# Kernel tuning notes

Hardware: AMD Instinct MI355X
Metric: run time of the kernel (lower is better)

## Reference

```python
import jax, jax.numpy as jnp
import numpy as np

B, N, E, H = 8, 512, 256, 8
HD = E // H
FF = 4 * E
TOPK = max(1, int(N * 0.2))
FW_MAX_DIST = 10      # default of get_shortest_path_matrix
EMB_MAX_IDX = 6       # spd encoder: max_dist(5) + 1
LN_EPS = 1e-5


def _layernorm(x, g, b):
    m = jnp.mean(x, axis=-1, keepdims=True)
    v = jnp.var(x, axis=-1, keepdims=True)
    return (x - m) / jnp.sqrt(v + LN_EPS) * g + b


def setup_inputs() -> dict:
    key = jax.random.key(0)
    ks = jax.random.split(key, 12)
    s = 0.02
    return {
        "x": jax.random.normal(ks[0], (B, N, E), jnp.float32),
        "adj": jax.random.uniform(ks[1], (B, N, N), jnp.float32),
        "emb_spd": (jax.random.normal(ks[2], (EMB_MAX_IDX + 1, H), jnp.float32) * s),
        "w_qkv": jax.random.normal(ks[3], (3 * E, E), jnp.float32) * s,
        "b_qkv": jnp.zeros((3 * E,), jnp.float32),
        "w_out": jax.random.normal(ks[4], (E, E), jnp.float32) * s,
        "b_out": jnp.zeros((E,), jnp.float32),
        "w_ff1": jax.random.normal(ks[5], (FF, E), jnp.float32) * s,
        "b_ff1": jnp.zeros((FF,), jnp.float32),
        "w_ff2": jax.random.normal(ks[6], (E, FF), jnp.float32) * s,
        "b_ff2": jnp.zeros((E,), jnp.float32),
        "g1": jnp.ones((E,), jnp.float32),
        "beta1": jnp.zeros((E,), jnp.float32),
        "g2": jnp.ones((E,), jnp.float32),
        "beta2": jnp.zeros((E,), jnp.float32),
        "w_pool": jax.random.normal(ks[7], (1, E), jnp.float32) * s,
        "b_pool": jnp.zeros((1,), jnp.float32),
    }


def _combined_mask(adj, emb_spd):
    # top-k per row -> binary adjacency via scatter
    _, idx = jax.lax.top_k(adj, TOPK)                       # [B,N,k]
    bi = jnp.arange(B)[:, None, None]
    ri = jnp.arange(N)[None, :, None]
    binary = jnp.zeros_like(adj).at[bi, ri, idx].set(1.0)   # [B,N,N]

    # Floyd-Warshall shortest paths
    dist = jnp.where(binary == 1.0, 1.0, jnp.inf)
    ids = jnp.arange(N)
    dist = dist.at[:, ids, ids].set(0.0)

    def body(k, d):
        return jnp.minimum(d, d[:, :, k][:, :, None] + d[:, k, :][:, None, :])

    dist = jax.lax.fori_loop(0, N, body, dist)
    dist_i = jnp.where(dist > FW_MAX_DIST, -1.0, dist).astype(jnp.int32)

    # spatial bias embedding: indices = clamp(dist+1, 0, max_dist+1)
    sp_idx = jnp.clip(dist_i + 1, 0, EMB_MAX_IDX)           # [B,N,N]
    bias = jnp.transpose(emb_spd[sp_idx], (0, 3, 1, 2))     # [B,H,N,N]

    base = jnp.where(binary == 0.0, -jnp.inf, 0.0)[:, None] # [B,1,N,N]
    return base + bias                                      # [B,H,N,N]


def reference(x, adj, emb_spd, w_qkv, b_qkv, w_out, b_out,
              w_ff1, b_ff1, w_ff2, b_ff2, g1, beta1, g2, beta2,
              w_pool, b_pool):
    mask = _combined_mask(adj, emb_spd)                     # [B,H,N,N]

    # multi-head self-attention (PyTorch MHA, post-norm encoder layer, eval)
    qkv = x @ w_qkv.T + b_qkv                               # [B,N,3E]
    q, k, v = jnp.split(qkv, 3, axis=-1)
    q = q.reshape(B, N, H, HD).transpose(0, 2, 1, 3)
    k = k.reshape(B, N, H, HD).transpose(0, 2, 1, 3)
    v = v.reshape(B, N, H, HD).transpose(0, 2, 1, 3)
    scores = jnp.einsum("bhqd,bhkd->bhqk", q, k) / np.sqrt(HD) + mask
    attn = jax.nn.softmax(scores, axis=-1)
    ctx = jnp.einsum("bhqk,bhkd->bhqd", attn, v)
    ctx = ctx.transpose(0, 2, 1, 3).reshape(B, N, E)
    attn_out = ctx @ w_out.T + b_out

    x1 = _layernorm(x + attn_out, g1, beta1)
    ff = jax.nn.relu(x1 @ w_ff1.T + b_ff1) @ w_ff2.T + b_ff2
    x2 = _layernorm(x1 + ff, g2, beta2)

    # attention pooling over nodes
    w = jax.nn.softmax(jnp.tanh(x2 @ w_pool.T + b_pool), axis=1)  # [B,N,1]
    return jnp.sum(x2 * w, axis=1)                          # [B,E]
```

## Files before the change

kernel.cpp:

```cpp
#include <hip/hip_runtime.h>
#include <math.h>


#define B_ 8
#define N_ 512
#define E_ 256
#define H_ 8
#define HD_ 32
#define TOPK_ 102

typedef __attribute__((ext_vector_type(8))) short bf16x8;
typedef __attribute__((ext_vector_type(4))) float f32x4;

__device__ __forceinline__ unsigned short f2b(float f) {
  unsigned u = __builtin_bit_cast(unsigned, f);
  return (unsigned short)((u + 0x7FFFu + ((u >> 16) & 1u)) >> 16);
}

__device__ __forceinline__ uint4 lnpack(const float* __restrict__ p,
                                        const float* __restrict__ g,
                                        const float* __restrict__ b,
                                        float mean, float inv) {
  float4 v0 = *(const float4*)p, v1 = *(const float4*)(p + 4);
  float4 g0 = *(const float4*)g, g1 = *(const float4*)(g + 4);
  float4 b0 = *(const float4*)b, b1 = *(const float4*)(b + 4);
  unsigned short h0 = f2b((v0.x - mean) * inv * g0.x + b0.x);
  unsigned short h1 = f2b((v0.y - mean) * inv * g0.y + b0.y);
  unsigned short h2 = f2b((v0.z - mean) * inv * g0.z + b0.z);
  unsigned short h3 = f2b((v0.w - mean) * inv * g0.w + b0.w);
  unsigned short h4 = f2b((v1.x - mean) * inv * g1.x + b1.x);
  unsigned short h5 = f2b((v1.y - mean) * inv * g1.y + b1.y);
  unsigned short h6 = f2b((v1.z - mean) * inv * g1.z + b1.z);
  unsigned short h7 = f2b((v1.w - mean) * inv * g1.w + b1.w);
  uint4 u;
  u.x = (unsigned)h0 | ((unsigned)h1 << 16);
  u.y = (unsigned)h2 | ((unsigned)h3 << 16);
  u.z = (unsigned)h4 | ((unsigned)h5 << 16);
  u.w = (unsigned)h6 | ((unsigned)h7 << 16);
  return u;
}

__global__ __launch_bounds__(256) void cvt_topk(
    const float* __restrict__ adj, unsigned int* __restrict__ bits,
    const float* __restrict__ x, const float* __restrict__ wqkv,
    const float* __restrict__ wout, const float* __restrict__ wff1,
    const float* __restrict__ wff2, unsigned short* __restrict__ xb,
    unsigned short* __restrict__ wqkvb, unsigned short* __restrict__ woutb,
    unsigned short* __restrict__ wff1b, unsigned short* __restrict__ wff2b,
    float* __restrict__ rstat) {
  __shared__ unsigned int hist[1024];
  __shared__ float cval[64];
  __shared__ int cidx[64];
  __shared__ int s_cnt, s_bb, s_need;
  __shared__ unsigned int rowbits[16];
  __shared__ int wsum[4];
  const int t = threadIdx.x;

  if (blockIdx.x >= 5888) {
    int i4 = (blockIdx.x - 5888) * 1024 + t * 4;
    *(float4*)(rstat + i4) = (float4){0.f, 0.f, 0.f, 0.f};
    return;
  }
  if (blockIdx.x >= 4096) {
    int i = ((blockIdx.x - 4096) * 256 + t) * 4;
    const float* src;
    unsigned short* dst;
    int off;
    if (i < 1048576)      { src = x;    dst = xb;    off = i; }
    else if (i < 1245184) { src = wqkv; dst = wqkvb; off = i - 1048576; }
    else if (i < 1310720) { src = wout; dst = woutb; off = i - 1245184; }
    else if (i < 1572864) { src = wff1; dst = wff1b; off = i - 1310720; }
    else                  { src = wff2; dst = wff2b; off = i - 1572864; }
    float4 v = *(const float4*)(src + off);
    ushort4 o;
    o.x = f2b(v.x); o.y = f2b(v.y); o.z = f2b(v.z); o.w = f2b(v.w);
    *(ushort4*)(dst + off) = o;
    return;
  }
  const int row = blockIdx.x;
  const float* a = adj + (size_t)row * N_;
  const int lane = t & 63;
  const int wave = t >> 6;

  hist[t] = 0u; hist[t + 256] = 0u; hist[t + 512] = 0u; hist[t + 768] = 0u;
  if (t == 0) s_cnt = 0;
  float v0 = a[t];
  float v1 = a[t + 256];
  __syncthreads();
  const int b0 = min(1023, max(0, (int)(v0 * 1024.0f)));
  const int b1 = min(1023, max(0, (int)(v1 * 1024.0f)));
  atomicAdd(&hist[b0], 1u);
  atomicAdd(&hist[b1], 1u);
  __syncthreads();
  const int base = 1020 - 4 * t;
  const int h0 = (int)hist[base], h1 = (int)hist[base + 1];
  const int h2 = (int)hist[base + 2], h3 = (int)hist[base + 3];
  const int g = h0 + h1 + h2 + h3;
  int sc = g;
  #pragma unroll
  for (int off = 1; off < 64; off <<= 1) {
    int y = __shfl_up(sc, off);
    sc += (lane >= off) ? y : 0;
  }
  if (lane == 63) wsum[wave] = sc;
  __syncthreads();
  int wo = 0;
  for (int w = 0; w < wave; w++) wo += wsum[w];
  const int incl = sc + wo;
  const int excl = incl - g;
  if (excl < TOPK_ && incl >= TOPK_) {
    int cum = excl;
    int bb = base;
    const int hh[4] = {h3, h2, h1, h0};
    const int bs[4] = {base + 3, base + 2, base + 1, base};
    #pragma unroll
    for (int u = 0; u < 4; u++) {
      if (cum + hh[u] >= TOPK_) { bb = bs[u]; break; }
      cum += hh[u];
    }
    s_bb = bb;
    s_need = TOPK_ - cum;
  }
  __syncthreads();
  const int bb = s_bb;
  const int need = s_need;
  const bool sel0 = (b0 > bb);
  const bool sel1 = (b1 > bb);
  if (b0 == bb) { int p = atomicAdd(&s_cnt, 1); if (p < 64) { cval[p] = v0; cidx[p] = t; } }
  if (b1 == bb) { int p = atomicAdd(&s_cnt, 1); if (p < 64) { cval[p] = v1; cidx[p] = t + 256; } }
  unsigned long long m0 = __ballot(sel0);
  unsigned long long m1 = __ballot(sel1);
  if (lane == 0) {
    rowbits[2 * wave + 0] = (unsigned int)m0;
    rowbits[2 * wave + 1] = (unsigned int)(m0 >> 32);
    rowbits[8 + 2 * wave + 0] = (unsigned int)m1;
    rowbits[8 + 2 * wave + 1] = (unsigned int)(m1 >> 32);
  }
  __syncthreads();
  const int cnt = min(s_cnt, 64);
  for (int c = t; c < cnt; c += 256) {
    const float v = cval[c];
    const int idx = cidx[c];
    int r = 0;
    for (int j = 0; j < cnt; j++) {
      const float vj = cval[j];
      const int ij = cidx[j];
      if (vj > v || (vj == v && ij < idx)) r++;
    }
    if (r < need) atomicOr(&rowbits[idx >> 5], 1u << (idx & 31));
  }
  __syncthreads();
  if (t < 16) bits[(size_t)row * 16 + t] = rowbits[t];
}

template <int FLAGS>
__global__ __launch_bounds__(256) void gemm_mfma(
    const unsigned short* __restrict__ A, const float* __restrict__ A32,
    const unsigned short* __restrict__ W, const float* __restrict__ bias,
    const float* __restrict__ res, void* __restrict__ Cout,
    unsigned short* __restrict__ kG, unsigned short* __restrict__ vG,
    float* __restrict__ rstat, const float* __restrict__ lng,
    const float* __restrict__ lnb, int M, int N, int K) {
  __shared__ __align__(16) unsigned short Af[8 * 64 * 8];
  __shared__ __align__(16) unsigned short Wf[8 * 64 * 8];
  const int tid = threadIdx.x;
  const int m0 = blockIdx.y * 64, n0 = blockIdx.x * 64;
  const int wave = tid >> 6, lane = tid & 63;
  const int wm = wave & 1, wn = wave >> 1;
  const int q = lane >> 4, l15 = lane & 15;
  const int r = tid >> 2, c0 = tid & 3;

  f32x4 acc[2][2];
  #pragma unroll
  for (int i = 0; i < 2; i++)
    #pragma unroll
    for (int j = 0; j < 2; j++) acc[i][j] = (f32x4){0.f, 0.f, 0.f, 0.f};

  float lmean = 0.f, linv = 0.f;
  if (FLAGS & 16) {
    float s = rstat[(size_t)(m0 + r) * 2];
    float s2 = rstat[(size_t)(m0 + r) * 2 + 1];
    lmean = s * (1.f / 256.f);
    float var = s2 * (1.f / 256.f) - lmean * lmean;
    linv = rsqrtf(var + 1e-5f);
  }

  const size_t arow = (size_t)(m0 + r) * K;
  const size_t wrow = (size_t)(n0 + r) * K;
  for (int k0 = 0; k0 < K; k0 += 64) {
    uint4 a0, a1;
    if (FLAGS & 16) {
      a0 = lnpack(A32 + arow + k0 + c0 * 8, lng + k0 + c0 * 8,
                  lnb + k0 + c0 * 8, lmean, linv);
      a1 = lnpack(A32 + arow + k0 + (c0 + 4) * 8, lng + k0 + (c0 + 4) * 8,
                  lnb + k0 + (c0 + 4) * 8, lmean, linv);
    } else {
      a0 = *(const uint4*)(A + arow + k0 + c0 * 8);
      a1 = *(const uint4*)(A + arow + k0 + (c0 + 4) * 8);
    }
    uint4 w0 = *(const uint4*)(W + wrow + k0 + c0 * 8);
    uint4 w1 = *(const uint4*)(W + wrow + k0 + (c0 + 4) * 8);
    __syncthreads();
    {
      int kc = c0 >> 2, qq = c0 & 3;
      int s0 = ((r >> 4) * 2 + kc) * 64 + (r & 15) + qq * 16;
      int kc1 = (c0 + 4) >> 2, qq1 = (c0 + 4) & 3;
      int s1 = ((r >> 4) * 2 + kc1) * 64 + (r & 15) + qq1 * 16;
      *(uint4*)(Af + s0 * 8) = a0;
      *(uint4*)(Af + s1 * 8) = a1;
      *(uint4*)(Wf + s0 * 8) = w0;
      *(uint4*)(Wf + s1 * 8) = w1;
    }
    __syncthreads();
    #pragma unroll
    for (int kc = 0; kc < 2; kc++) {
      bf16x8 af[2], wf[2];
      #pragma unroll
      for (int mt = 0; mt < 2; mt++)
        af[mt] = *(const bf16x8*)(Af + (((wm * 2 + mt) * 2 + kc) * 64 + lane) * 8);
      #pragma unroll
      for (int nt = 0; nt < 2; nt++)
        wf[nt] = *(const bf16x8*)(Wf + (((wn * 2 + nt) * 2 + kc) * 64 + lane) * 8);
      #pragma unroll
      for (int mt = 0; mt < 2; mt++)
        #pragma unroll
        for (int nt = 0; nt < 2; nt++)
          acc[mt][nt] = __builtin_amdgcn_mfma_f32_16x16x32_bf16(af[mt], wf[nt], acc[mt][nt], 0, 0, 0);
    }
  }
  float srow[2][4], sqrow[2][4];
  if (FLAGS & 8) {
    #pragma unroll
    for (int mt = 0; mt < 2; mt++)
      #pragma unroll
      for (int reg = 0; reg < 4; reg++) { srow[mt][reg] = 0.f; sqrow[mt][reg] = 0.f; }
  }
  #pragma unroll
  for (int nt = 0; nt < 2; nt++) {
    const int col = n0 + (wn * 2 + nt) * 16 + l15;
    const float bv = bias[col];
    #pragma unroll
    for (int mt = 0; mt < 2; mt++) {
      const int rowb = m0 + (wm * 2 + mt) * 16 + q * 4;
      float ov[4];
      #pragma unroll
      for (int reg = 0; reg < 4; reg++) {
        float o = acc[mt][nt][reg] + bv;
        if (res) {
          float rv = res[(size_t)(rowb + reg) * N + col];
          if (FLAGS & 32) {
            const int rr = rowb + reg;
            float s = rstat[(size_t)rr * 2];
            float s2 = rstat[(size_t)rr * 2 + 1];
            float mn = s * (1.f / 256.f);
            float vv = s2 * (1.f / 256.f) - mn * mn;
            float iv = rsqrtf(vv + 1e-5f);
            rv = (rv - mn) * iv * lng[col] + lnb[col];
          }
          o += rv;
        }
        if (FLAGS & 1) o = fmaxf(o, 0.f);
        if (FLAGS & 8) { srow[mt][reg] += o; sqrow[mt][reg] += o * o; }
        ov[reg] = o;
      }
      if (FLAGS & 4) {
        if (col < 256) {
          #pragma unroll
          for (int reg = 0; reg < 4; reg++)
            ((unsigned short*)Cout)[(size_t)(rowb + reg) * 256 + col] = f2b(ov[reg]);
        } else if (col < 512) {
          const int dfull = col - 256;
          const int hh2 = dfull >> 5, d = dfull & 31;
          const int q2 = d >> 3, sub = d & 7;
          const int bidx = rowb >> 9, j = rowb & 511;
          const int jt = j >> 6, jtile = (j >> 4) & 3, jl = j & 15;
          unsigned short* kp = kG +
              ((size_t)(((bidx * 8 + hh2) * 8 + jt) * 4 + jtile) * 64 + q2 * 16 + jl) * 8 + sub;
          kp[0] = f2b(ov[0]); kp[8] = f2b(ov[1]); kp[16] = f2b(ov[2]); kp[24] = f2b(ov[3]);
        } else {
          const int dfull = col - 512;
          const int hh2 = dfull >> 5, d = dfull & 31;
          const int dt = d >> 4, dl = d & 15;
          const int bidx = rowb >> 9, j = rowb & 511;
          const int jt = j >> 6, jj = j & 63;
          const int kc = jj >> 5, q2 = (jj >> 3) & 3, sub0 = jj & 7;
          ushort4 st;
          st.x = f2b(ov[0]); st.y = f2b(ov[1]); st.z = f2b(ov[2]); st.w = f2b(ov[3]);
          *(ushort4*)(vG +
              ((size_t)(((bidx * 8 + hh2) * 8 + jt) * 4 + dt * 2 + kc) * 64 + q2 * 16 + dl) * 8 + sub0) = st;
        }
      } else if (FLAGS & 2) {
        #pragma unroll
        for (int reg = 0; reg < 4; reg++)
          ((unsigned short*)Cout)[(size_t)(rowb + reg) * N + col] = f2b(ov[reg]);
      } else {
        #pragma unroll
        for (int reg = 0; reg < 4; reg++)
          ((float*)Cout)[(size_t)(rowb + reg) * N + col] = ov[reg];
      }
    }
  }
  if (FLAGS & 8) {
    #pragma unroll
    for (int mt = 0; mt < 2; mt++)
      #pragma unroll
      for (int reg = 0; reg < 4; reg++) {
        float s = srow[mt][reg], s2 = sqrow[mt][reg];
        #pragma unroll
        for (int off = 1; off < 16; off <<= 1) {
          s += __shfl_xor(s, off);
          s2 += __shfl_xor(s2, off);
        }
        if (l15 == 0) {
          const int row = m0 + (wm * 2 + mt) * 16 + q * 4 + reg;
          atomicAdd(&rstat[(size_t)row * 2], s);
          atomicAdd(&rstat[(size_t)row * 2 + 1], s2);
        }
      }
  }
}

__global__ __launch_bounds__(256) void attn_mfma(
    const unsigned short* __restrict__ qb, const unsigned short* __restrict__ kG,
    const unsigned short* __restrict__ vG, const unsigned int* __restrict__ bits,
    const float* __restrict__ emb, unsigned short* __restrict__ ctxo) {
  const int bx = blockIdx.x;
  const int ib = bx & 7;
  const int h = (bx >> 3) & 7;
  const int b = bx >> 6;
  const int tid = threadIdx.x;
  const int lane = tid & 63;
  const int wave = tid >> 6;
  const int q = lane >> 4, l15 = lane & 15;

  __shared__ __align__(16) unsigned int mrow[64 * 16];
  __shared__ __align__(16) unsigned short pF[4][2 * 64 * 8];

  {
    int rr = tid >> 2, wq = tid & 3;
    uint4 mw = *(const uint4*)(bits + ((size_t)(b * N_ + ib * 64 + rr)) * 16 + wq * 4);
    *(uint4*)(mrow + rr * 16 + wq * 4) = mw;
  }
  __syncthreads();

  const int i0w = ib * 64 + wave * 16;
  const bf16x8 qf = *(const bf16x8*)(qb + ((size_t)(b * N_ + i0w + l15)) * 256 + h * HD_ + q * 8);
  const float delta = emb[1 * H_ + h] - emb[2 * H_ + h];
  const float scale = 0.17677669529663687f;

  float m_run[4], l_run[4];
  #pragma unroll
  for (int e = 0; e < 4; e++) { m_run[e] = -1e30f; l_run[e] = 0.f; }
  f32x4 cacc[2];
  cacc[0] = (f32x4){0.f, 0.f, 0.f, 0.f};
  cacc[1] = (f32x4){0.f, 0.f, 0.f, 0.f};

  unsigned short* pbase = &pF[wave][0];
  const unsigned short* kb = kG + (size_t)(b * 8 + h) * 8 * 4 * 512;
  const unsigned short* vb = vG + (size_t)(b * 8 + h) * 8 * 4 * 512;

  #pragma unroll 1
  for (int jt = 0; jt < 8; jt++) {
    f32x4 s4[4];
    #pragma unroll
    for (int jtile = 0; jtile < 4; jtile++) {
      bf16x8 kf = *(const bf16x8*)(kb + (size_t)(jt * 4 + jtile) * 512 + lane * 8);
      s4[jtile] = __builtin_amdgcn_mfma_f32_16x16x32_bf16(qf, kf, (f32x4){0.f, 0.f, 0.f, 0.f}, 0, 0, 0);
    }
    unsigned long long mw64[4];
    #pragma unroll
    for (int reg = 0; reg < 4; reg++)
      mw64[reg] = *(const unsigned long long*)(mrow + (wave * 16 + q * 4 + reg) * 16 + jt * 2);
    float smat[4][4];
    #pragma unroll
    for (int jtile = 0; jtile < 4; jtile++) {
      #pragma unroll
      for (int reg = 0; reg < 4; reg++) {
        unsigned int w = (jtile & 2) ? (unsigned int)(mw64[reg] >> 32) : (unsigned int)mw64[reg];
        bool allowed = ((w >> ((jtile & 1) * 16 + l15)) & 1u) != 0u;
        int ig = ib * 64 + wave * 16 + q * 4 + reg;
        int jg = jt * 64 + jtile * 16 + l15;
        float s = s4[jtile][reg] * scale + ((jg == ig) ? delta : 0.f);
        smat[jtile][reg] = allowed ? s : -INFINITY;
      }
    }
    float alpha[4], pmat[4][4];
    #pragma unroll
    for (int reg = 0; reg < 4; reg++) {
      float mloc = fmaxf(fmaxf(smat[0][reg], smat[1][reg]), fmaxf(smat[2][reg], smat[3][reg]));
      #pragma unroll
      for (int off = 1; off < 16; off <<= 1) mloc = fmaxf(mloc, __shfl_xor(mloc, off));
      float mnew = fmaxf(m_run[reg], mloc);
      alpha[reg] = __expf(m_run[reg] - mnew);
      m_run[reg] = mnew;
      float ps = 0.f;
      #pragma unroll
      for (int jtile = 0; jtile < 4; jtile++) {
        float p = __expf(smat[jtile][reg] - mnew);
        pmat[jtile][reg] = p;
        ps += p;
      }
      #pragma unroll
      for (int off = 1; off < 16; off <<= 1) ps += __shfl_xor(ps, off);
      l_run[reg] = l_run[reg] * alpha[reg] + ps;
      cacc[0][reg] *= alpha[reg];
      cacc[1][reg] *= alpha[reg];
    }
    #pragma unroll
    for (int jtile = 0; jtile < 4; jtile++) {
      int j_l = jtile * 16 + l15;
      int sl = ((j_l >> 5) * 64 + ((j_l >> 3) & 3) * 16) * 8 + (j_l & 7);
      #pragma unroll
      for (int reg = 0; reg < 4; reg++)
        pbase[sl + (q * 4 + reg) * 8] = f2b(pmat[jtile][reg]);
    }
    #pragma unroll
    for (int kc = 0; kc < 2; kc++) {
      bf16x8 pf = *(const bf16x8*)(pbase + (kc * 64 + lane) * 8);
      #pragma unroll
      for (int dt = 0; dt < 2; dt++) {
        bf16x8 vf = *(const bf16x8*)(vb + (size_t)(jt * 4 + dt * 2 + kc) * 512 + lane * 8);
        cacc[dt] = __builtin_amdgcn_mfma_f32_16x16x32_bf16(pf, vf, cacc[dt], 0, 0, 0);
      }
    }
  }
  #pragma unroll
  for (int reg = 0; reg < 4; reg++) {
    const float linv = 1.f / l_run[reg];
    const size_t row = (size_t)(b * N_ + i0w + q * 4 + reg);
    #pragma unroll
    for (int dt = 0; dt < 2; dt++)
      ctxo[row * E_ + h * HD_ + dt * 16 + l15] = f2b(cacc[dt][reg] * linv);
  }
}

__global__ __launch_bounds__(256) void ln2pool_kernel(
    const float* __restrict__ t, const float* __restrict__ g,
    const float* __restrict__ be, const float* __restrict__ wp,
    const float* __restrict__ bp, float* __restrict__ partial,
    float* __restrict__ pwsum) {
  __shared__ float sh[8];
  const int tid = threadIdx.x;
  const int wave = tid >> 6, lane = tid & 63;
  const int c = blockIdx.x;
  const float gv = g[tid], bev = be[tid], wpv = wp[tid], bpv = bp[0];
  float pacc = 0.f, esum = 0.f;
  #pragma unroll 1
  for (int rr = 0; rr < 8; rr++) {
    const int row = c * 8 + rr;
    float v = t[(size_t)row * E_ + tid];
    float s = v, s2 = v * v;
    #pragma unroll
    for (int off = 32; off > 0; off >>= 1) {
      s += __shfl_xor(s, off);
      s2 += __shfl_xor(s2, off);
    }
    __syncthreads();
    if (lane == 0) { sh[wave] = s; sh[4 + wave] = s2; }
    __syncthreads();
    s = sh[0] + sh[1] + sh[2] + sh[3];
    s2 = sh[4] + sh[5] + sh[6] + sh[7];
    float mean = s * (1.f / 256.f);
    float var = s2 * (1.f / 256.f) - mean * mean;
    float inv = rsqrtf(var + 1e-5f);
    float o = (v - mean) * inv * gv + bev;
    float d = o * wpv;
    #pragma unroll
    for (int off = 32; off > 0; off >>= 1) d += __shfl_xor(d, off);
    __syncthreads();
    if (lane == 0) sh[wave] = d;
    __syncthreads();
    float dot = sh[0] + sh[1] + sh[2] + sh[3] + bpv;
    float e = __expf(tanhf(dot));
    pacc += e * o;
    esum += e;
  }
  partial[(size_t)c * E_ + tid] = pacc;
  if (tid == 0) pwsum[c] = esum;
}

__global__ __launch_bounds__(256) void pool_final(
    const float* __restrict__ partial, const float* __restrict__ pwsum,
    float* __restrict__ out) {
  const int b = blockIdx.x;
  const int tid = threadIdx.x;
  float acc = 0.f, ws = 0.f;
  #pragma unroll
  for (int c = 0; c < 64; c++) acc += partial[(size_t)(b * 64 + c) * E_ + tid];
  #pragma unroll
  for (int c = 0; c < 64; c++) ws += pwsum[b * 64 + c];
  out[b * E_ + tid] = acc / ws;
}

extern "C" void kernel_launch(void* const* d_in, const int* in_sizes, int n_in,
                              void* d_out, int out_size, void* d_ws, size_t ws_size,
                              hipStream_t stream) {
  (void)in_sizes; (void)n_in; (void)out_size; (void)ws_size;
  const float* x      = (const float*)d_in[0];
  const float* adj    = (const float*)d_in[1];
  const float* emb    = (const float*)d_in[2];
  const float* w_qkv  = (const float*)d_in[3];
  const float* b_qkv  = (const float*)d_in[4];
  const float* w_out  = (const float*)d_in[5];
  const float* b_out  = (const float*)d_in[6];
  const float* w_ff1  = (const float*)d_in[7];
  const float* b_ff1  = (const float*)d_in[8];
  const float* w_ff2  = (const float*)d_in[9];
  const float* b_ff2  = (const float*)d_in[10];
  const float* g1     = (const float*)d_in[11];
  const float* be1    = (const float*)d_in[12];
  const float* g2     = (const float*)d_in[13];
  const float* be2    = (const float*)d_in[14];
  const float* w_pool = (const float*)d_in[15];
  const float* b_pool = (const float*)d_in[16];

  char* ws = (char*)d_ws;
  unsigned int*   bits  = (unsigned int*)ws;
  unsigned short* xb    = (unsigned short*)(ws + 262144);
  unsigned short* qb    = (unsigned short*)(ws + 2359296);
  unsigned short* kG    = (unsigned short*)(ws + 4456448);
  unsigned short* vG    = (unsigned short*)(ws + 6553600);
  unsigned short* ctxb  = (unsigned short*)(ws + 8650752);
  float*          tbuf  = (float*)(ws + 10747904);
  float*          tbuf2 = (float*)(ws + 14942208);
  float*          rstat = (float*)(ws + 19136512);
  unsigned short* hffb  = (unsigned short*)(ws + 21233664);
  unsigned short* wqkvb = (unsigned short*)(ws + 29622272);
  unsigned short* woutb = (unsigned short*)(ws + 30015488);
  unsigned short* wff1b = (unsigned short*)(ws + 30146560);
  unsigned short* wff2b = (unsigned short*)(ws + 30670848);
  float*          partial = (float*)(ws + 31195136);
  float*          pwsum   = (float*)(ws + 31719424);
  float*          outp  = (float*)d_out;

  const int M = B_ * N_;

  cvt_topk<<<4096 + 1792 + 2, 256, 0, stream>>>(
      adj, bits, x, w_qkv, w_out, w_ff1, w_ff2, xb, wqkvb, woutb, wff1b,
      wff2b, rstat);
  gemm_mfma<4><<<dim3(768 / 64, M / 64), 256, 0, stream>>>(
      xb, nullptr, wqkvb, b_qkv, nullptr, qb, kG, vG, nullptr, nullptr,
      nullptr, M, 768, E_);
  attn_mfma<<<B_ * H_ * (N_ / 64), 256, 0, stream>>>(qb, kG, vG, bits, emb, ctxb);
  gemm_mfma<8><<<dim3(E_ / 64, M / 64), 256, 0, stream>>>(
      ctxb, nullptr, woutb, b_out, x, tbuf, nullptr, nullptr, rstat, nullptr,
      nullptr, M, E_, E_);
  gemm_mfma<1 | 2 | 16><<<dim3(1024 / 64, M / 64), 256, 0, stream>>>(
      nullptr, tbuf, wff1b, b_ff1, nullptr, hffb, nullptr, nullptr, rstat,
      g1, be1, M, 1024, E_);
  gemm_mfma<32><<<dim3(E_ / 64, M / 64), 256, 0, stream>>>(
      hffb, nullptr, wff2b, b_ff2, tbuf, tbuf2, nullptr, nullptr, rstat,
      g1, be1, M, E_, 1024);
  ln2pool_kernel<<<M / 8, 256, 0, stream>>>(tbuf2, g2, be2, w_pool, b_pool,
                                            partial, pwsum);
  pool_final<<<B_, 256, 0, stream>>>(partial, pwsum, outp);
}
```

Before: 175.5 us.

## Use direct global-to-LDS loads in GEMM tiles and per-wave row pooling

The GEMM's bf16 A and W tile loads now use global_load_lds, so data goes straight from global memory into shared memory instead of passing through registers. The LDS layout is kept through per-lane address mapping. Runtime flag checks become if constexpr, and the residual path is gated by a new template bit rather than a null-pointer test. The LN2-plus-pool kernel now gives each wave whole rows with float4 loads and wave-level reductions, cutting the block barriers per row to a single final barrier. The risk is getting the LDS address mapping wrong for global_load_lds, and the GEMM still has no double buffering.

```diff
diff --git a/kernel.cpp b/kernel.cpp
--- a/kernel.cpp
+++ b/kernel.cpp
@@ -15,6 +15,12 @@
 __device__ __forceinline__ unsigned short f2b(float f) {
   unsigned u = __builtin_bit_cast(unsigned, f);
   return (unsigned short)((u + 0x7FFFu + ((u >> 16) & 1u)) >> 16);
+}
+
+__device__ __forceinline__ void gload16(const void* g, void* l) {
+  __builtin_amdgcn_global_load_lds(
+      (const __attribute__((address_space(1))) void*)g,
+      (__attribute__((address_space(3))) void*)l, 16, 0, 0);
 }
 
 __device__ __forceinline__ uint4 lnpack(const float* __restrict__ p,
@@ -177,7 +183,7 @@
     for (int j = 0; j < 2; j++) acc[i][j] = (f32x4){0.f, 0.f, 0.f, 0.f};
 
   float lmean = 0.f, linv = 0.f;
-  if (FLAGS & 16) {
+  if constexpr (FLAGS & 16) {
     float s = rstat[(size_t)(m0 + r) * 2];
     float s2 = rstat[(size_t)(m0 + r) * 2 + 1];
     lmean = s * (1.f / 256.f);
@@ -185,32 +191,45 @@
     linv = rsqrtf(var + 1e-5f);
   }
 
+  const int rl = lane & 15;
+  const int colk = ((wave & 1) << 5) + ((lane >> 4) << 3);
+  const unsigned short* wp0 =
+      W + (size_t)(n0 + ((wave >> 1) << 4) + rl) * K + colk;
+  const unsigned short* wp1 = wp0 + (size_t)32 * K;
+  unsigned short* ldsW0 = Wf + (size_t)(wave * 64) * 8;
+  unsigned short* ldsW1 = Wf + (size_t)(256 + wave * 64) * 8;
+  const unsigned short* ap0 = nullptr;
+  const unsigned short* ap1 = nullptr;
+  unsigned short* ldsA0 = Af + (size_t)(wave * 64) * 8;
+  unsigned short* ldsA1 = Af + (size_t)(256 + wave * 64) * 8;
+  if constexpr (!(FLAGS & 16)) {
+    ap0 = A + (size_t)(m0 + ((wave >> 1) << 4) + rl) * K + colk;
+    ap1 = ap0 + (size_t)32 * K;
+  }
+
   const size_t arow = (size_t)(m0 + r) * K;
-  const size_t wrow = (size_t)(n0 + r) * K;
   for (int k0 = 0; k0 < K; k0 += 64) {
     uint4 a0, a1;
-    if (FLAGS & 16) {
+    if constexpr (FLAGS & 16) {
       a0 = lnpack(A32 + arow + k0 + c0 * 8, lng + k0 + c0 * 8,
                   lnb + k0 + c0 * 8, lmean, linv);
       a1 = lnpack(A32 + arow + k0 + (c0 + 4) * 8, lng + k0 + (c0 + 4) * 8,
                   lnb + k0 + (c0 + 4) * 8, lmean, linv);
-    } else {
-      a0 = *(const uint4*)(A + arow + k0 + c0 * 8);
-      a1 = *(const uint4*)(A + arow + k0 + (c0 + 4) * 8);
-    }
-    uint4 w0 = *(const uint4*)(W + wrow + k0 + c0 * 8);
-    uint4 w1 = *(const uint4*)(W + wrow + k0 + (c0 + 4) * 8);
+    }
     __syncthreads();
-    {
+    if constexpr (FLAGS & 16) {
       int kc = c0 >> 2, qq = c0 & 3;
       int s0 = ((r >> 4) * 2 + kc) * 64 + (r & 15) + qq * 16;
       int kc1 = (c0 + 4) >> 2, qq1 = (c0 + 4) & 3;
       int s1 = ((r >> 4) * 2 + kc1) * 64 + (r & 15) + qq1 * 16;
       *(uint4*)(Af + s0 * 8) = a0;
       *(uint4*)(Af + s1 * 8) = a1;
-      *(uint4*)(Wf + s0 * 8) = w0;
-      *(uint4*)(Wf + s1 * 8) = w1;
-    }
+    } else {
+      gload16(ap0 + k0, ldsA0);
+      gload16(ap1 + k0, ldsA1);
+    }
+    gload16(wp0 + k0, ldsW0);
+    gload16(wp1 + k0, ldsW1);
     __syncthreads();
     #pragma unroll
     for (int kc = 0; kc < 2; kc++) {
@@ -229,7 +248,7 @@
     }
   }
   float srow[2][4], sqrow[2][4];
-  if (FLAGS & 8) {
+  if constexpr (FLAGS & 8) {
     #pragma unroll
     for (int mt = 0; mt < 2; mt++)
       #pragma unroll
@@ -246,9 +265,9 @@
       #pragma unroll
       for (int reg = 0; reg < 4; reg++) {
         float o = acc[mt][nt][reg] + bv;
-        if (res) {
+        if constexpr (FLAGS & 64) {
           float rv = res[(size_t)(rowb + reg) * N + col];
-          if (FLAGS & 32) {
+          if constexpr (FLAGS & 32) {
             const int rr = rowb + reg;
             float s = rstat[(size_t)rr * 2];
             float s2 = rstat[(size_t)rr * 2 + 1];
@@ -259,11 +278,11 @@
           }
           o += rv;
         }
-        if (FLAGS & 1) o = fmaxf(o, 0.f);
-        if (FLAGS & 8) { srow[mt][reg] += o; sqrow[mt][reg] += o * o; }
+        if constexpr (FLAGS & 1) o = fmaxf(o, 0.f);
+        if constexpr (FLAGS & 8) { srow[mt][reg] += o; sqrow[mt][reg] += o * o; }
         ov[reg] = o;
       }
-      if (FLAGS & 4) {
+      if constexpr (FLAGS & 4) {
         if (col < 256) {
           #pragma unroll
           for (int reg = 0; reg < 4; reg++)
@@ -289,7 +308,7 @@
           *(ushort4*)(vG +
               ((size_t)(((bidx * 8 + hh2) * 8 + jt) * 4 + dt * 2 + kc) * 64 + q2 * 16 + dl) * 8 + sub0) = st;
         }
-      } else if (FLAGS & 2) {
+      } else if constexpr (FLAGS & 2) {
         #pragma unroll
         for (int reg = 0; reg < 4; reg++)
           ((unsigned short*)Cout)[(size_t)(rowb + reg) * N + col] = f2b(ov[reg]);
@@ -300,7 +319,7 @@
       }
     }
   }
-  if (FLAGS & 8) {
+  if constexpr (FLAGS & 8) {
     #pragma unroll
     for (int mt = 0; mt < 2; mt++)
       #pragma unroll
@@ -439,44 +458,50 @@
     const float* __restrict__ be, const float* __restrict__ wp,
     const float* __restrict__ bp, float* __restrict__ partial,
     float* __restrict__ pwsum) {
-  __shared__ float sh[8];
+  __shared__ float sh[4][256];
+  __shared__ float she[4];
   const int tid = threadIdx.x;
   const int wave = tid >> 6, lane = tid & 63;
   const int c = blockIdx.x;
-  const float gv = g[tid], bev = be[tid], wpv = wp[tid], bpv = bp[0];
-  float pacc = 0.f, esum = 0.f;
-  #pragma unroll 1
-  for (int rr = 0; rr < 8; rr++) {
-    const int row = c * 8 + rr;
-    float v = t[(size_t)row * E_ + tid];
-    float s = v, s2 = v * v;
-    #pragma unroll
-    for (int off = 32; off > 0; off >>= 1) {
+  const int col = lane * 4;
+  const float4 gv = *(const float4*)(g + col);
+  const float4 bev = *(const float4*)(be + col);
+  const float4 wpv = *(const float4*)(wp + col);
+  const float bpv = bp[0];
+  float4 pacc = {0.f, 0.f, 0.f, 0.f};
+  float esum = 0.f;
+  #pragma unroll
+  for (int rr = 0; rr < 2; rr++) {
+    const int row = c * 8 + wave * 2 + rr;
+    float4 v = *(const float4*)(t + (size_t)row * E_ + col);
+    float s = v.x + v.y + v.z + v.w;
+    float s2 = v.x * v.x + v.y * v.y + v.z * v.z + v.w * v.w;
+    #pragma unroll
+    for (int off = 1; off < 64; off <<= 1) {
       s += __shfl_xor(s, off);
       s2 += __shfl_xor(s2, off);
     }
-    __syncthreads();
-    if (lane == 0) { sh[wave] = s; sh[4 + wave] = s2; }
-    __syncthreads();
-    s = sh[0] + sh[1] + sh[2] + sh[3];
-    s2 = sh[4] + sh[5] + sh[6] + sh[7];
     float mean = s * (1.f / 256.f);
     float var = s2 * (1.f / 256.f) - mean * mean;
     float inv = rsqrtf(var + 1e-5f);
-    float o = (v - mean) * inv * gv + bev;
-    float d = o * wpv;
-    #pragma unroll
-    for (int off = 32; off > 0; off >>= 1) d += __shfl_xor(d, off);
-    __syncthreads();
-    if (lane == 0) sh[wave] = d;
-    __syncthreads();
-    float dot = sh[0] + sh[1] + sh[2] + sh[3] + bpv;
-    float e = __expf(tanhf(dot));
-    pacc += e * o;
+    float4 o;
+    o.x = (v.x - mean) * inv * gv.x + bev.x;
+    o.y = (v.y - mean) * inv * gv.y + bev.y;
+    o.z = (v.z - mean) * inv * gv.z + bev.z;
+    o.w = (v.w - mean) * inv * gv.w + bev.w;
+    float d = o.x * wpv.x + o.y * wpv.y + o.z * wpv.z + o.w * wpv.w;
+    #pragma unroll
+    for (int off = 1; off < 64; off <<= 1) d += __shfl_xor(d, off);
+    float e = __expf(tanhf(d + bpv));
+    pacc.x += e * o.x; pacc.y += e * o.y; pacc.z += e * o.z; pacc.w += e * o.w;
     esum += e;
   }
-  partial[(size_t)c * E_ + tid] = pacc;
-  if (tid == 0) pwsum[c] = esum;
+  *(float4*)(&sh[wave][col]) = pacc;
+  if (lane == 0) she[wave] = esum;
+  __syncthreads();
+  partial[(size_t)c * E_ + tid] =
+      sh[0][tid] + sh[1][tid] + sh[2][tid] + sh[3][tid];
+  if (tid == 0) pwsum[c] = she[0] + she[1] + she[2] + she[3];
 }
 
 __global__ __launch_bounds__(256) void pool_final(
@@ -542,13 +567,13 @@
       xb, nullptr, wqkvb, b_qkv, nullptr, qb, kG, vG, nullptr, nullptr,
       nullptr, M, 768, E_);
   attn_mfma<<<B_ * H_ * (N_ / 64), 256, 0, stream>>>(qb, kG, vG, bits, emb, ctxb);
-  gemm_mfma<8><<<dim3(E_ / 64, M / 64), 256, 0, stream>>>(
+  gemm_mfma<8 | 64><<<dim3(E_ / 64, M / 64), 256, 0, stream>>>(
       ctxb, nullptr, woutb, b_out, x, tbuf, nullptr, nullptr, rstat, nullptr,
       nullptr, M, E_, E_);
   gemm_mfma<1 | 2 | 16><<<dim3(1024 / 64, M / 64), 256, 0, stream>>>(
       nullptr, tbuf, wff1b, b_ff1, nullptr, hffb, nullptr, nullptr, rstat,
       g1, be1, M, 1024, E_);
-  gemm_mfma<32><<<dim3(E_ / 64, M / 64), 256, 0, stream>>>(
+  gemm_mfma<32 | 64><<<dim3(E_ / 64, M / 64), 256, 0, stream>>>(
       hffb, nullptr, wff2b, b_ff2, tbuf, tbuf2, nullptr, nullptr, rstat,
       g1, be1, M, E_, 1024);
   ln2pool_kernel<<<M / 8, 256, 0, stream>>>(tbuf2, g2, be2, w_pool, b_pool,
```

After: 171.5 us. -2.3%, faster.
